# Kernel tuning notes

Measured on AMD Instinct MI355X. Metric: run time of the kernel, lower is better.

The kernel has to match this reference:

```python
import jax, jax.numpy as jnp
import numpy as np

N_SRC = 200000
N_EDGES = 1280000
N_SEG = 100000
D = 64


def setup_inputs() -> dict:
    key = jax.random.key(0)
    k1, k2, k3 = jax.random.split(key, 3)
    values = jax.random.normal(k1, (N_SRC, D), dtype=jnp.float32)
    gather_idx = jax.random.randint(k2, (N_EDGES,), 0, N_SRC, dtype=jnp.int64)
    segment_ids = jnp.sort(jax.random.randint(k3, (N_EDGES,), 0, N_SEG, dtype=jnp.int64))
    return {
        "values": values,
        "gather_idx": gather_idx,
        "segment_ids": segment_ids,
        "num_segments": N_SEG,
    }


def reference(values, gather_idx, segment_ids, num_segments):
    # AGG_GATHER: indexed gather of input values  -> [E, D]
    gathered = values[gather_idx]
    # AGG_SCATTER_REDUCE: scatter_mean over ragged segments (sorted ids)
    sums = jax.ops.segment_sum(gathered, segment_ids, num_segments=num_segments,
                               indices_are_sorted=True)
    counts = jax.ops.segment_sum(jnp.ones((gathered.shape[0],), dtype=values.dtype),
                                 segment_ids, num_segments=num_segments,
                                 indices_are_sorted=True)
    # mean = sum / count (guard empty segments)
    return sums / jnp.maximum(counts, 1.0)[:, None]
```

## Files before the change

### kernel.cpp

```cpp
#include <hip/hip_runtime.h>


#define D 64

typedef float  f4v __attribute__((ext_vector_type(4)));

__global__ __launch_bounds__(256) void prep_kernel(
    const float* __restrict__ src,
    unsigned short* __restrict__ dst,
    const int* __restrict__ segment_ids,
    int*       __restrict__ starts,
    int n, int n_padded,
    int n_edges, int n_seg,
    int cvt_blocks)
{
    if ((int)blockIdx.x < cvt_blocks) {
        const int i = (blockIdx.x * blockDim.x + threadIdx.x) * 8;
        if (i >= n_padded) return;
        float4 a = make_float4(0.f, 0.f, 0.f, 0.f);
        float4 b = make_float4(0.f, 0.f, 0.f, 0.f);
        if (i < n) {
            a = *(const float4*)(src + i);
            b = *(const float4*)(src + i + 4);
        }
        #define PACK_BF16(x, y) ({                                     \
            unsigned ux = __float_as_uint(x);                          \
            unsigned uy = __float_as_uint(y);                          \
            ux = (ux + 0x7FFFu + ((ux >> 16) & 1u)) >> 16;             \
            uy = (uy + 0x7FFFu + ((uy >> 16) & 1u)) >> 16;             \
            ux | (uy << 16); })
        uint4 o;
        o.x = PACK_BF16(a.x, a.y);
        o.y = PACK_BF16(a.z, a.w);
        o.z = PACK_BF16(b.x, b.y);
        o.w = PACK_BF16(b.z, b.w);
        #undef PACK_BF16
        *(uint4*)(dst + i) = o;
    } else {
        const int e       = (blockIdx.x - cvt_blocks) * blockDim.x + threadIdx.x;
        const bool active = (e < n_edges);
        const int ec      = active ? e : (n_edges - 1);
        const int s       = segment_ids[ec];
        const int lane    = threadIdx.x & 63;
        int sprev         = __shfl_up(s, 1, 64);
        if (lane == 0) sprev = (ec == 0) ? -1 : segment_ids[ec - 1];
        if (active) {
            for (int t = sprev + 1; t <= s; ++t) starts[t] = e;
            if (e == n_edges - 1) {
                for (int t = s + 1; t <= n_seg; ++t) starts[t] = n_edges;
            }
        }
    }
}

__global__ __launch_bounds__(256) void seg_mean_bf16_kernel(
    const unsigned short* __restrict__ vals16,
    const int*   __restrict__ gather_idx,
    const int*   __restrict__ starts,
    float*       __restrict__ out,
    int n_seg, int n_src)
{
    const int wave = (blockIdx.x * blockDim.x + threadIdx.x) >> 6;
    const int lane = threadIdx.x & 63;
    const int s0 = wave << 1;
    if (s0 >= n_seg) return;
    const int s1 = s0 + 1;
    const bool has1 = (s1 < n_seg);

    const int sub = lane >> 4;
    const int cg  = lane & 15;

    const int st0 = __builtin_nontemporal_load(starts + s0);
    const int en0 = __builtin_nontemporal_load(starts + s0 + 1);
    const int st1 = en0;
    const int en1 = has1 ? __builtin_nontemporal_load(starts + s1 + 1) : en0;

    const uint2* __restrict__ rows = (const uint2*)vals16;

    float4 acc0 = make_float4(0.f, 0.f, 0.f, 0.f);
    float4 acc1 = make_float4(0.f, 0.f, 0.f, 0.f);

    int b0 = st0, b1 = st1;
    while (b0 < en0 || b1 < en1) {
        const int ea0 = b0 + 0  + sub, ea1 = b0 + 4  + sub;
        const int ea2 = b0 + 8  + sub, ea3 = b0 + 12 + sub;
        const int eb0 = b1 + 0  + sub, eb1 = b1 + 4  + sub;
        const int eb2 = b1 + 8  + sub, eb3 = b1 + 12 + sub;
        const bool ma0 = ea0 < en0, ma1 = ea1 < en0, ma2 = ea2 < en0, ma3 = ea3 < en0;
        const bool mb0 = eb0 < en1, mb1 = eb1 < en1, mb2 = eb2 < en1, mb3 = eb3 < en1;
        const int ia0 = ma0 ? gather_idx[ea0] : n_src;
        const int ia1 = ma1 ? gather_idx[ea1] : n_src;
        const int ia2 = ma2 ? gather_idx[ea2] : n_src;
        const int ia3 = ma3 ? gather_idx[ea3] : n_src;
        const int ib0 = mb0 ? gather_idx[eb0] : n_src;
        const int ib1 = mb1 ? gather_idx[eb1] : n_src;
        const int ib2 = mb2 ? gather_idx[eb2] : n_src;
        const int ib3 = mb3 ? gather_idx[eb3] : n_src;
        const uint2 va0 = rows[((long long)ia0 << 4) + cg];
        const uint2 va1 = rows[((long long)ia1 << 4) + cg];
        const uint2 va2 = rows[((long long)ia2 << 4) + cg];
        const uint2 va3 = rows[((long long)ia3 << 4) + cg];
        const uint2 vb0 = rows[((long long)ib0 << 4) + cg];
        const uint2 vb1 = rows[((long long)ib1 << 4) + cg];
        const uint2 vb2 = rows[((long long)ib2 << 4) + cg];
        const uint2 vb3 = rows[((long long)ib3 << 4) + cg];
        #define ACC(A, V)                                              \
            A.x += __uint_as_float((V).x << 16);                       \
            A.y += __uint_as_float((V).x & 0xFFFF0000u);               \
            A.z += __uint_as_float((V).y << 16);                       \
            A.w += __uint_as_float((V).y & 0xFFFF0000u);
        ACC(acc0, va0) ACC(acc0, va1) ACC(acc0, va2) ACC(acc0, va3)
        ACC(acc1, vb0) ACC(acc1, vb1) ACC(acc1, vb2) ACC(acc1, vb3)
        #undef ACC
        b0 += 16; b1 += 16;
    }

    acc0.x += __shfl_xor(acc0.x, 16, 64); acc0.y += __shfl_xor(acc0.y, 16, 64);
    acc0.z += __shfl_xor(acc0.z, 16, 64); acc0.w += __shfl_xor(acc0.w, 16, 64);
    acc0.x += __shfl_xor(acc0.x, 32, 64); acc0.y += __shfl_xor(acc0.y, 32, 64);
    acc0.z += __shfl_xor(acc0.z, 32, 64); acc0.w += __shfl_xor(acc0.w, 32, 64);
    acc1.x += __shfl_xor(acc1.x, 16, 64); acc1.y += __shfl_xor(acc1.y, 16, 64);
    acc1.z += __shfl_xor(acc1.z, 16, 64); acc1.w += __shfl_xor(acc1.w, 16, 64);
    acc1.x += __shfl_xor(acc1.x, 32, 64); acc1.y += __shfl_xor(acc1.y, 32, 64);
    acc1.z += __shfl_xor(acc1.z, 32, 64); acc1.w += __shfl_xor(acc1.w, 32, 64);

    const int c0 = en0 - st0;
    const int c1 = en1 - st1;
    const float inv0 = (c0 > 0) ? (1.0f / (float)c0) : 1.0f;
    const float inv1 = (c1 > 0) ? (1.0f / (float)c1) : 1.0f;

    if (sub == 0 || (sub == 1 && has1)) {
        f4v r;
        if (sub == 0) {
            r.x = acc0.x * inv0; r.y = acc0.y * inv0;
            r.z = acc0.z * inv0; r.w = acc0.w * inv0;
        } else {
            r.x = acc1.x * inv1; r.y = acc1.y * inv1;
            r.z = acc1.z * inv1; r.w = acc1.w * inv1;
        }
        const int s = s0 + sub;
        __builtin_nontemporal_store(r, (f4v*)(out + ((long long)s << 6) + (cg << 2)));
    }
}

__global__ __launch_bounds__(256) void seg_mean_bsearch_kernel(
    const float* __restrict__ values,
    const int*   __restrict__ gather_idx,
    const int*   __restrict__ segment_ids,
    float*       __restrict__ out,
    int n_edges, int n_seg)
{
    const int wave = (blockIdx.x * blockDim.x + threadIdx.x) >> 6;
    const int lane = threadIdx.x & 63;
    if (wave >= n_seg) return;
    const int s = wave;
    int lo = 0, hi = n_edges;
    while (lo < hi) { int mid = (lo + hi) >> 1; if (segment_ids[mid] < s) lo = mid + 1; else hi = mid; }
    const int start = lo;
    hi = n_edges;
    while (lo < hi) { int mid = (lo + hi) >> 1; if (segment_ids[mid] < s + 1) lo = mid + 1; else hi = mid; }
    const int end = lo;
    float sum = 0.0f;
    for (int e = start; e < end; ++e) sum += values[((long long)gather_idx[e] << 6) + lane];
    const int count = end - start;
    const float inv = (count > 0) ? (1.0f / (float)count) : 1.0f;
    out[((long long)s << 6) + lane] = sum * inv;
}

extern "C" void kernel_launch(void* const* d_in, const int* in_sizes, int n_in,
                              void* d_out, int out_size, void* d_ws, size_t ws_size,
                              hipStream_t stream) {
    const float* values      = (const float*)d_in[0];
    const int*   gather_idx  = (const int*)d_in[1];
    const int*   segment_ids = (const int*)d_in[2];
    float* out = (float*)d_out;

    const int n_values = in_sizes[0];
    const int n_edges  = in_sizes[1];
    const int n_seg    = out_size / D;
    const int n_src    = n_values / D;

    const int    n_padded    = n_values + D;
    const size_t table_bytes = (size_t)n_padded * sizeof(unsigned short);
    const size_t starts_off  = (table_bytes + 15) & ~(size_t)15;
    const size_t need        = starts_off + (size_t)(n_seg + 1) * sizeof(int);

    if (ws_size >= need) {
        unsigned short* vals16 = (unsigned short*)d_ws;
        int* starts = (int*)((char*)d_ws + starts_off);
        {
            const int threads    = 256;
            const int cvt_blocks = (n_padded / 8 + threads - 1) / threads;
            const int st_blocks  = (n_edges + threads - 1) / threads;
            prep_kernel<<<cvt_blocks + st_blocks, threads, 0, stream>>>(
                values, vals16, segment_ids, starts,
                n_values, n_padded, n_edges, n_seg, cvt_blocks);
        }
        {
            const int n_waves = (n_seg + 1) >> 1;
            const int threads = 256;
            const int blocks  = (n_waves * 64 + threads - 1) / threads;
            seg_mean_bf16_kernel<<<blocks, threads, 0, stream>>>(
                vals16, gather_idx, starts, out, n_seg, n_src);
        }
    } else {
        const int threads = 256;
        const int blocks  = (n_seg * 64 + threads - 1) / threads;
        seg_mean_bsearch_kernel<<<blocks, threads, 0, stream>>>(
            values, gather_idx, segment_ids, out, n_edges, n_seg);
    }
}
```

Baseline: 135.8 us.

## Process one segment per wave with 16-byte row loads and eight edges per pass

The mean kernel now gives each wave a single segment instead of two interleaved ones. Each lane loads a 16-byte chunk (8 bf16 values), so eight lanes cover a row and eight edges are in flight per step, with two steps per loop iteration. Gather-index loads are clamped and marked nontemporal, and the reduction now takes three shuffle stages. This doubles the wave count and halves the per-wave memory-level parallelism compared with the old eight-rows-in-flight scheme, trading latency hiding per wave for wider loads and simpler control flow.

Measured after the change: 142.2 us. 1.05x slower.

```diff
diff --git a/kernel.cpp b/kernel.cpp
--- a/kernel.cpp
+++ b/kernel.cpp
@@ -3,7 +3,7 @@
 
 #define D 64
 
-typedef float  f4v __attribute__((ext_vector_type(4)));
+typedef float f4v __attribute__((ext_vector_type(4)));
 
 __global__ __launch_bounds__(256) void prep_kernel(
     const float* __restrict__ src,
@@ -62,84 +62,56 @@
 {
     const int wave = (blockIdx.x * blockDim.x + threadIdx.x) >> 6;
     const int lane = threadIdx.x & 63;
-    const int s0 = wave << 1;
-    if (s0 >= n_seg) return;
-    const int s1 = s0 + 1;
-    const bool has1 = (s1 < n_seg);
+    if (wave >= n_seg) return;
 
-    const int sub = lane >> 4;
-    const int cg  = lane & 15;
+    const int sub = lane >> 3;
+    const int c8  = lane & 7;
 
-    const int st0 = __builtin_nontemporal_load(starts + s0);
-    const int en0 = __builtin_nontemporal_load(starts + s0 + 1);
-    const int st1 = en0;
-    const int en1 = has1 ? __builtin_nontemporal_load(starts + s1 + 1) : en0;
+    const int start = __builtin_nontemporal_load(starts + wave);
+    const int end   = __builtin_nontemporal_load(starts + wave + 1);
 
-    const uint2* __restrict__ rows = (const uint2*)vals16;
+    const uint4* __restrict__ rows = (const uint4*)vals16;
 
-    float4 acc0 = make_float4(0.f, 0.f, 0.f, 0.f);
-    float4 acc1 = make_float4(0.f, 0.f, 0.f, 0.f);
+    float a[8] = {0.f, 0.f, 0.f, 0.f, 0.f, 0.f, 0.f, 0.f};
 
-    int b0 = st0, b1 = st1;
-    while (b0 < en0 || b1 < en1) {
-        const int ea0 = b0 + 0  + sub, ea1 = b0 + 4  + sub;
-        const int ea2 = b0 + 8  + sub, ea3 = b0 + 12 + sub;
-        const int eb0 = b1 + 0  + sub, eb1 = b1 + 4  + sub;
-        const int eb2 = b1 + 8  + sub, eb3 = b1 + 12 + sub;
-        const bool ma0 = ea0 < en0, ma1 = ea1 < en0, ma2 = ea2 < en0, ma3 = ea3 < en0;
-        const bool mb0 = eb0 < en1, mb1 = eb1 < en1, mb2 = eb2 < en1, mb3 = eb3 < en1;
-        const int ia0 = ma0 ? gather_idx[ea0] : n_src;
-        const int ia1 = ma1 ? gather_idx[ea1] : n_src;
-        const int ia2 = ma2 ? gather_idx[ea2] : n_src;
-        const int ia3 = ma3 ? gather_idx[ea3] : n_src;
-        const int ib0 = mb0 ? gather_idx[eb0] : n_src;
-        const int ib1 = mb1 ? gather_idx[eb1] : n_src;
-        const int ib2 = mb2 ? gather_idx[eb2] : n_src;
-        const int ib3 = mb3 ? gather_idx[eb3] : n_src;
-        const uint2 va0 = rows[((long long)ia0 << 4) + cg];
-        const uint2 va1 = rows[((long long)ia1 << 4) + cg];
-        const uint2 va2 = rows[((long long)ia2 << 4) + cg];
-        const uint2 va3 = rows[((long long)ia3 << 4) + cg];
-        const uint2 vb0 = rows[((long long)ib0 << 4) + cg];
-        const uint2 vb1 = rows[((long long)ib1 << 4) + cg];
-        const uint2 vb2 = rows[((long long)ib2 << 4) + cg];
-        const uint2 vb3 = rows[((long long)ib3 << 4) + cg];
-        #define ACC(A, V)                                              \
-            A.x += __uint_as_float((V).x << 16);                       \
-            A.y += __uint_as_float((V).x & 0xFFFF0000u);               \
-            A.z += __uint_as_float((V).y << 16);                       \
-            A.w += __uint_as_float((V).y & 0xFFFF0000u);
-        ACC(acc0, va0) ACC(acc0, va1) ACC(acc0, va2) ACC(acc0, va3)
-        ACC(acc1, vb0) ACC(acc1, vb1) ACC(acc1, vb2) ACC(acc1, vb3)
-        #undef ACC
-        b0 += 16; b1 += 16;
+    for (int base = start; base < end; base += 16) {
+        const int e0  = base + sub;
+        const int e1  = base + 8 + sub;
+        const int ec0 = (e0 < end) ? e0 : (end - 1);
+        const int ec1 = (e1 < end) ? e1 : (end - 1);
+        int i0 = __builtin_nontemporal_load(gather_idx + ec0);
+        int i1 = __builtin_nontemporal_load(gather_idx + ec1);
+        i0 = (e0 < end) ? i0 : n_src;
+        i1 = (e1 < end) ? i1 : n_src;
+        const uint4 v0 = rows[((long long)i0 << 3) + c8];
+        const uint4 v1 = rows[((long long)i1 << 3) + c8];
+        a[0] += __uint_as_float(v0.x << 16); a[1] += __uint_as_float(v0.x & 0xFFFF0000u);
+        a[2] += __uint_as_float(v0.y << 16); a[3] += __uint_as_float(v0.y & 0xFFFF0000u);
+        a[4] += __uint_as_float(v0.z << 16); a[5] += __uint_as_float(v0.z & 0xFFFF0000u);
+        a[6] += __uint_as_float(v0.w << 16); a[7] += __uint_as_float(v0.w & 0xFFFF0000u);
+        a[0] += __uint_as_float(v1.x << 16); a[1] += __uint_as_float(v1.x & 0xFFFF0000u);
+        a[2] += __uint_as_float(v1.y << 16); a[3] += __uint_as_float(v1.y & 0xFFFF0000u);
+        a[4] += __uint_as_float(v1.z << 16); a[5] += __uint_as_float(v1.z & 0xFFFF0000u);
+        a[6] += __uint_as_float(v1.w << 16); a[7] += __uint_as_float(v1.w & 0xFFFF0000u);
     }
 
-    acc0.x += __shfl_xor(acc0.x, 16, 64); acc0.y += __shfl_xor(acc0.y, 16, 64);
-    acc0.z += __shfl_xor(acc0.z, 16, 64); acc0.w += __shfl_xor(acc0.w, 16, 64);
-    acc0.x += __shfl_xor(acc0.x, 32, 64); acc0.y += __shfl_xor(acc0.y, 32, 64);
-    acc0.z += __shfl_xor(acc0.z, 32, 64); acc0.w += __shfl_xor(acc0.w, 32, 64);
-    acc1.x += __shfl_xor(acc1.x, 16, 64); acc1.y += __shfl_xor(acc1.y, 16, 64);
-    acc1.z += __shfl_xor(acc1.z, 16, 64); acc1.w += __shfl_xor(acc1.w, 16, 64);
-    acc1.x += __shfl_xor(acc1.x, 32, 64); acc1.y += __shfl_xor(acc1.y, 32, 64);
-    acc1.z += __shfl_xor(acc1.z, 32, 64); acc1.w += __shfl_xor(acc1.w, 32, 64);
+    #pragma unroll
+    for (int k = 0; k < 8; ++k) {
+        a[k] += __shfl_xor(a[k], 8, 64);
+        a[k] += __shfl_xor(a[k], 16, 64);
+        a[k] += __shfl_xor(a[k], 32, 64);
+    }
 
-    const int c0 = en0 - st0;
-    const int c1 = en1 - st1;
-    const float inv0 = (c0 > 0) ? (1.0f / (float)c0) : 1.0f;
-    const float inv1 = (c1 > 0) ? (1.0f / (float)c1) : 1.0f;
+    const int count = end - start;
+    const float inv = (count > 0) ? (1.0f / (float)count) : 1.0f;
 
-    if (sub == 0 || (sub == 1 && has1)) {
-        f4v r;
-        if (sub == 0) {
-            r.x = acc0.x * inv0; r.y = acc0.y * inv0;
-            r.z = acc0.z * inv0; r.w = acc0.w * inv0;
-        } else {
-            r.x = acc1.x * inv1; r.y = acc1.y * inv1;
-            r.z = acc1.z * inv1; r.w = acc1.w * inv1;
-        }
-        const int s = s0 + sub;
-        __builtin_nontemporal_store(r, (f4v*)(out + ((long long)s << 6) + (cg << 2)));
+    if (sub == 0) {
+        f4v r0, r1;
+        r0.x = a[0] * inv; r0.y = a[1] * inv; r0.z = a[2] * inv; r0.w = a[3] * inv;
+        r1.x = a[4] * inv; r1.y = a[5] * inv; r1.z = a[6] * inv; r1.w = a[7] * inv;
+        float* p = out + ((long long)wave << 6) + (c8 << 3);
+        __builtin_nontemporal_store(r0, (f4v*)p);
+        __builtin_nontemporal_store(r1, (f4v*)(p + 4));
     }
 }
 
@@ -197,9 +169,8 @@
                 n_values, n_padded, n_edges, n_seg, cvt_blocks);
         }
         {
-            const int n_waves = (n_seg + 1) >> 1;
             const int threads = 256;
-            const int blocks  = (n_waves * 64 + threads - 1) / threads;
+            const int blocks  = (n_seg * 64 + threads - 1) / threads;
             seg_mean_bf16_kernel<<<blocks, threads, 0, stream>>>(
                 vals16, gather_idx, starts, out, n_seg, n_src);
         }
```
